# Optimization experiments

Hardware: AMD Instinct MI355X
Metric: run time of the kernel (lower is better)

The kernel has to match this reference:

```python
import jax, jax.numpy as jnp
import numpy as np

N_WIRES = 8
N_LAYERS = 6
OUTPUT_DIM = 8
BATCH = 131072


def _rx(t):
    c = jnp.cos(t / 2).astype(jnp.complex64)
    s = jnp.sin(t / 2).astype(jnp.complex64)
    return jnp.stack([jnp.stack([c, -1j * s], -1), jnp.stack([-1j * s, c], -1)], -2)


def _ry(t):
    c = jnp.cos(t / 2).astype(jnp.complex64)
    s = jnp.sin(t / 2).astype(jnp.complex64)
    return jnp.stack([jnp.stack([c, -s], -1), jnp.stack([s, c], -1)], -2)


def _rz(t):
    e = jnp.exp(-0.5j * t.astype(jnp.complex64))
    z = jnp.zeros_like(e)
    return jnp.stack([jnp.stack([e, z], -1), jnp.stack([z, jnp.conj(e)], -1)], -2)


def _apply_1q(state, U, w):
    # state: [B, 2, 2, ..., 2]; U: [2,2] (shared) or [B,2,2] (per-batch angle)
    s = jnp.moveaxis(state, w + 1, -1)
    if U.ndim == 3:
        s = jnp.einsum('bij,b...j->b...i', U, s)
    else:
        s = jnp.einsum('ij,...j->...i', U, s)
    return jnp.moveaxis(s, -1, w + 1)


def _apply_cnot(state, c, t):
    s = jnp.moveaxis(state, (c + 1, t + 1), (-2, -1))
    s = jnp.concatenate([s[..., :1, :], s[..., 1:, ::-1]], axis=-2)
    return jnp.moveaxis(s, (-2, -1), (c + 1, t + 1))


def _circuit(x, weights):
    B = x.shape[0]
    dim = 2 ** N_WIRES
    state = jnp.zeros((B, dim), dtype=jnp.complex64).at[:, 0].set(1.0)
    state = state.reshape((B,) + (2,) * N_WIRES)
    rx0 = _rx(x[:, 0])  # [B,2,2] data-encoding gates (batched angles)
    ry1 = _ry(x[:, 1])
    for layer in range(N_LAYERS):
        for i in range(N_WIRES):
            state = _apply_1q(state, rx0 if i % 2 == 0 else ry1, i)
        for i in range(N_WIRES):
            state = _apply_1q(state, _rx(weights[layer, i, 0]), i)
            state = _apply_1q(state, _ry(weights[layer, i, 1]), i)
            state = _apply_1q(state, _rz(weights[layer, i, 2]), i)
        for i in range(N_WIRES - 1):
            state = _apply_cnot(state, i, i + 1)
    probs = state.real ** 2 + state.imag ** 2  # [B, 2,...,2]
    evs = []
    for i in range(OUTPUT_DIM):
        p = jnp.moveaxis(probs, i + 1, 1).reshape(B, 2, -1)
        evs.append((p[:, 0] - p[:, 1]).sum(-1))  # <Z_i>
    return jnp.stack(evs, 0)  # [output_dim, B]


def setup_inputs() -> dict:
    key = jax.random.key(0)
    k1, k2 = jax.random.split(key)
    x = jax.random.normal(k1, (BATCH, 2), dtype=jnp.float32)
    weights = jax.random.normal(k2, (N_LAYERS, N_WIRES, 3), dtype=jnp.float32)
    return {'x': x, 'weights': weights}


def reference(x, weights):
    basis_t = _circuit(x, weights) * jnp.pi  # [output_dim, B]
    return basis_t.T  # [B, output_dim]
```

## Files before the change

### kernel.cpp

```cpp
#include <hip/hip_runtime.h>
#include <math.h>

#define N_WIRES 8
#define N_LAYERS 6
#define NG 49
#define NG2 (NG * NG)

#define WS_E_OFF 0
#define WS_FB_OFF 76832

typedef _Float16 half8 __attribute__((ext_vector_type(8)));
typedef float f32x4 __attribute__((ext_vector_type(4)));

__device__ __forceinline__ float row16_sum(float v) {
    v += __int_as_float(__builtin_amdgcn_update_dpp(
        0, __float_as_int(v), 0xB1, 0xF, 0xF, true));
    v += __int_as_float(__builtin_amdgcn_update_dpp(
        0, __float_as_int(v), 0x4E, 0xF, 0xF, true));
    v += __int_as_float(__builtin_amdgcn_update_dpp(
        0, __float_as_int(v), 0x124, 0xF, 0xF, true));
    v += __int_as_float(__builtin_amdgcn_update_dpp(
        0, __float_as_int(v), 0x128, 0xF, 0xF, true));
    return v;
}

__global__ __launch_bounds__(256) void qnn_grid_lds(const float* __restrict__ w,
                                                    float* __restrict__ E) {
    __shared__ float gates[N_LAYERS * N_WIRES * 8];
    __shared__ float2 bufA[256];
    __shared__ float2 bufB[256];
    __shared__ float partial[4][8];

    const int tid = threadIdx.x;
    const int g = blockIdx.x;
    const int ga = (g * 1338) >> 16;
    const int gb = g - ga * NG;
    const float step = (float)(2.0 * M_PI / 49.0);

    if (tid < N_LAYERS * N_WIRES) {
        const int i = tid & 7;
        float wx = w[tid * 3 + 0], wy = w[tid * 3 + 1], wz = w[tid * 3 + 2];
        float sx, cx, sy, cy, sz, cz;
        sincosf(0.5f * wx, &sx, &cx);
        sincosf(0.5f * wy, &sy, &cy);
        sincosf(0.5f * wz, &sz, &cz);
        float A00r = cy * cx, A00i = sy * sx;
        float A01r = -sy * cx, A01i = -cy * sx;
        float A10r = sy * cx, A10i = -cy * sx;
        float A11r = cy * cx, A11i = -sy * sx;
        float U00r = A00r * cz + A00i * sz, U00i = A00i * cz - A00r * sz;
        float U01r = A01r * cz + A01i * sz, U01i = A01i * cz - A01r * sz;
        float U10r = A10r * cz - A10i * sz, U10i = A10i * cz + A10r * sz;
        float U11r = A11r * cz - A11i * sz, U11i = A11i * cz + A11r * sz;
        float V00r, V00i, V01r, V01i, V10r, V10i, V11r, V11i;
        if ((i & 1) == 0) {
            V00r = U01i; V00i = -U01r;
            V01r = U00i; V01i = -U00r;
            V10r = U11i; V10i = -U11r;
            V11r = U10i; V11i = -U10r;
        } else {
            V00r = U01r;  V00i = U01i;
            V01r = -U00r; V01i = -U00i;
            V10r = U11r;  V10i = U11i;
            V11r = -U10r; V11i = -U10i;
        }
        const float xx = (i & 1) ? (step * (float)gb) : (step * (float)ga);
        float se, ce;
        sincosf(0.5f * xx, &se, &ce);
        float* o = gates + tid * 8;
        o[0] = ce * U00r + se * V00r;  o[1] = ce * U00i + se * V00i;
        o[2] = ce * U01r + se * V01r;  o[3] = ce * U01i + se * V01i;
        o[4] = ce * U10r + se * V10r;  o[5] = ce * U10i + se * V10i;
        o[6] = ce * U11r + se * V11r;  o[7] = ce * U11i + se * V11i;
    }

    float ar = (tid == 0) ? 1.0f : 0.0f;
    float ai = 0.0f;
    __syncthreads();

    int flip = 0;
    for (int l = 0; l < N_LAYERS; ++l) {
        #pragma unroll
        for (int i = 0; i < 2; ++i) {
            const float* gm = gates + (l * 8 + i) * 8;
            const int p = 7 - i;
            const int m = 1 << p;
            const int bit = (tid >> p) & 1;
            float2* buf = flip ? bufB : bufA;
            flip ^= 1;
            buf[tid] = make_float2(ar, ai);
            __syncthreads();
            float2 other = buf[tid ^ m];
            float a0r = bit ? other.x : ar, a0i = bit ? other.y : ai;
            float a1r = bit ? ar : other.x, a1i = bit ? ai : other.y;
            float c0r = gm[bit * 4 + 0], c0i = gm[bit * 4 + 1];
            float c1r = gm[bit * 4 + 2], c1i = gm[bit * 4 + 3];
            float nr = c0r * a0r - c0i * a0i + c1r * a1r - c1i * a1i;
            float ni = c0r * a0i + c0i * a0r + c1r * a1i + c1i * a1r;
            ar = nr; ai = ni;
        }
        #pragma unroll
        for (int i = 2; i < 8; ++i) {
            const float* gm = gates + (l * 8 + i) * 8;
            const int p = 7 - i;
            const int m = 1 << p;
            const int bit = (tid >> p) & 1;
            float otr = __shfl_xor(ar, m);
            float oti = __shfl_xor(ai, m);
            float a0r = bit ? otr : ar, a0i = bit ? oti : ai;
            float a1r = bit ? ar : otr, a1i = bit ? ai : oti;
            float c0r = gm[bit * 4 + 0], c0i = gm[bit * 4 + 1];
            float c1r = gm[bit * 4 + 2], c1i = gm[bit * 4 + 3];
            float nr = c0r * a0r - c0i * a0i + c1r * a1r - c1i * a1i;
            float ni = c0r * a0i + c0i * a0r + c1r * a1i + c1i * a1r;
            ar = nr; ai = ni;
        }
        {
            float2* buf = flip ? bufB : bufA;
            flip ^= 1;
            buf[tid] = make_float2(ar, ai);
            __syncthreads();
            float2 src = buf[tid ^ (tid >> 1)];
            ar = src.x; ai = src.y;
        }
    }

    float p = ar * ar + ai * ai;
    float ev[8];
    #pragma unroll
    for (int i = 0; i < 8; ++i) ev[i] = ((tid >> (7 - i)) & 1) ? -p : p;
    #pragma unroll
    for (int i = 0; i < 8; ++i) {
        float v = row16_sum(ev[i]);
        v += __shfl_xor(v, 16);
        v += __shfl_xor(v, 32);
        ev[i] = v;
    }
    const int wave = tid >> 6, lane = tid & 63;
    if (lane == 0) {
        #pragma unroll
        for (int i = 0; i < 8; ++i) partial[wave][i] = ev[i];
    }
    __syncthreads();
    if (tid < 8) {
        E[tid * NG2 + g] = partial[0][tid] + partial[1][tid] + partial[2][tid] + partial[3][tid];
    }
}

__global__ __launch_bounds__(64) void dft2(const float* __restrict__ E,
                                           _Float16* __restrict__ Fb) {
    const int kp = blockIdx.x, i = blockIdx.y, t = threadIdx.x;
    __shared__ float Es[NG2];
    __shared__ float H[NG];
    __shared__ float tc[NG], ts[NG];
    const float step = (float)(2.0 * M_PI / 49.0);
    const float PI = 3.14159265358979323846f;

    if (t < NG) {
        float s, c;
        sincosf(step * (float)t, &s, &c);
        tc[t] = c; ts[t] = s;
    }
    if (kp < NG) {
        for (int e = t; e < NG2; e += 64) Es[e] = E[i * NG2 + e];
    }
    __syncthreads();

    if (kp < NG && t < NG) {
        const int b = t;
        const int n = (kp + 1) >> 1;
        const bool use_cos = (kp & 1) || (kp == 0);
        float acc = 0.f;
        int j = 0;
        for (int a = 0; a < NG; ++a) {
            acc = fmaf(Es[a * NG + b], use_cos ? tc[j] : ts[j], acc);
            j += n; if (j >= NG) j -= NG;
        }
        acc *= (kp == 0) ? (1.0f / 49.0f) : (2.0f / 49.0f);
        H[b] = acc;
    }
    __syncthreads();

    const int l = t;
    float acc = 0.f;
    if (kp < NG && l < NG) {
        const int n = (l + 1) >> 1;
        const bool use_cos = (l & 1) || (l == 0);
        int j = 0;
        for (int b = 0; b < NG; ++b) {
            acc = fmaf(H[b], use_cos ? tc[j] : ts[j], acc);
            j += n; if (j >= NG) j -= NG;
        }
        acc *= (l == 0) ? (PI / 49.0f) : (2.0f * PI / 49.0f);
    }
    {
        const int ntile = kp >> 4, n = kp & 15;
        const int chunk = l >> 5, lrem = l & 31;
        const int q = lrem >> 3, j = lrem & 7;
        const int fid = (i * 4 + ntile) * 2 + chunk;
        Fb[fid * 512 + (q * 16 + n) * 8 + j] = (_Float16)acc;
    }
}

#define V0PAD 68

__global__ __launch_bounds__(256, 4) void contract_mfma(const float* __restrict__ x,
                                                        const _Float16* __restrict__ Fb,
                                                        float* __restrict__ out, int B) {
    __shared__ float xs0[64], xs1[64];
    __shared__ float v0t[64 * V0PAD];
    __shared__ __align__(16) half8 aS[2 * 4 * 64];

    const int tid = threadIdx.x;
    const int bbase = blockIdx.x * 64;
    if (bbase >= B) return;

    const int lane = tid & 63;
    const int w = tid >> 6;
    const int q = lane >> 4;

    const half8* FB = (const half8*)Fb;
    half8 bfrag[16];
    #pragma unroll
    for (int f = 0; f < 16; ++f) bfrag[f] = FB[(w * 16 + f) * 64 + lane];

    if (tid < 64) {
        float2 xv = ((const float2*)x)[bbase + tid];
        xs0[tid] = xv.x;
        xs1[tid] = xv.y;
    }
    __syncthreads();

    {
        const int b = tid & 63, s = tid >> 6;
        const float x0 = xs0[b];
        float c1, s1;
        sincosf(x0, &s1, &c1);
        float s2v = 2.f * s1 * c1, c2v = 1.f - 2.f * s1 * s1;
        float s4v = 2.f * s2v * c2v, c4v = 1.f - 2.f * s2v * s2v;
        float s8v = 2.f * s4v * c4v, c8v = 1.f - 2.f * s4v * s4v;
        float sb, cb;
        if (s == 0) {
            sb = 0.f; cb = 1.f;
        } else if (s == 1) {
            sb = s8v; cb = c8v;
        } else if (s == 2) {
            sb = 2.f * s8v * c8v; cb = 1.f - 2.f * s8v * s8v;
        } else {
            float s16v = 2.f * s8v * c8v, c16v = 1.f - 2.f * s8v * s8v;
            sb = s16v * c8v + c16v * s8v; cb = c16v * c8v - s16v * s8v;
        }
        float* row = v0t + b * V0PAD + 16 * s;
        const int k0 = 16 * s;
        row[0] = (k0 == 0) ? 1.0f : ((k0 < NG) ? sb : 0.0f);
        float cm = cb, sm = sb;
        #pragma unroll
        for (int j = 1; j < 16; ++j) {
            if (j & 1) {
                float c2 = cm * c1 - sm * s1, s2 = sm * c1 + cm * s1;
                cm = c2; sm = s2;
            }
            float val = (j & 1) ? cm : sm;
            row[j] = ((k0 + j) < NG) ? val : 0.0f;
        }
    }

    {
        const float x1v = xs1[w * 16 + (lane & 15)];
        float c1, s1;
        sincosf(x1v, &s1, &c1);
        float s2v = 2.f * s1 * c1, c2v = 1.f - 2.f * s1 * s1;
        float s4v = 2.f * s2v * c2v, c4v = 1.f - 2.f * s2v * s2v;
        float s8v = 2.f * s4v * c4v, c8v = 1.f - 2.f * s4v * s4v;
        float s12v = s8v * c4v + c8v * s4v, c12v = c8v * c4v - s8v * s4v;
        float sq = (q == 0) ? 0.f : ((q == 1) ? s4v : ((q == 2) ? s8v : s12v));
        float cq = (q == 0) ? 1.f : ((q == 1) ? c4v : ((q == 2) ? c8v : c12v));
        float s16v = 2.f * s8v * c8v, c16v = 1.f - 2.f * s8v * s8v;
        float sb_c[2], cb_c[2];
        sb_c[0] = sq;                      cb_c[0] = cq;
        sb_c[1] = sq * c16v + cq * s16v;   cb_c[1] = cq * c16v - sq * s16v;
        #pragma unroll
        for (int c = 0; c < 2; ++c) {
            const int l0 = c * 32 + q * 8;
            float cb = cb_c[c], sb = sb_c[c];
            float vals[8];
            vals[0] = (l0 == 0) ? 1.0f : sb;
            float cm = cb, sm = sb;
            #pragma unroll
            for (int j = 1; j < 8; ++j) {
                if (j & 1) {
                    float c2 = cm * c1 - sm * s1, s2 = sm * c1 + cm * s1;
                    cm = c2; sm = s2;
                }
                vals[j] = (j & 1) ? cm : sm;
            }
            half8 af;
            #pragma unroll
            for (int j = 0; j < 8; ++j) {
                af[j] = (_Float16)(((l0 + j) < 52) ? vals[j] : 0.0f);
            }
            aS[(c * 4 + w) * 64 + lane] = af;
        }
    }

    __syncthreads();

    #pragma unroll 1
    for (int bg = 0; bg < 4; ++bg) {
        const half8 a0 = aS[(0 * 4 + bg) * 64 + lane];
        const half8 a1 = aS[(1 * 4 + bg) * 64 + lane];

        float res[2][4];
        #pragma unroll
        for (int ii = 0; ii < 2; ++ii)
            #pragma unroll
            for (int r = 0; r < 4; ++r) res[ii][r] = 0.f;

        #pragma unroll
        for (int nt = 0; nt < 4; ++nt) {
            float v0[4];
            #pragma unroll
            for (int r = 0; r < 4; ++r)
                v0[r] = v0t[(bg * 16 + q * 4 + r) * V0PAD + nt * 16 + (lane & 15)];

            f32x4 z = {0.f, 0.f, 0.f, 0.f};
            f32x4 acc0 = __builtin_amdgcn_mfma_f32_16x16x32_f16(a0, bfrag[nt * 2 + 0], z, 0, 0, 0);
            acc0 = __builtin_amdgcn_mfma_f32_16x16x32_f16(a1, bfrag[nt * 2 + 1], acc0, 0, 0, 0);
            f32x4 acc1 = __builtin_amdgcn_mfma_f32_16x16x32_f16(a0, bfrag[(4 + nt) * 2 + 0], z, 0, 0, 0);
            acc1 = __builtin_amdgcn_mfma_f32_16x16x32_f16(a1, bfrag[(4 + nt) * 2 + 1], acc1, 0, 0, 0);

            #pragma unroll
            for (int r = 0; r < 4; ++r) {
                res[0][r] = fmaf(acc0[r], v0[r], res[0][r]);
                res[1][r] = fmaf(acc1[r], v0[r], res[1][r]);
            }
        }

        #pragma unroll
        for (int ii = 0; ii < 2; ++ii)
            #pragma unroll
            for (int r = 0; r < 4; ++r) {
                res[ii][r] = row16_sum(res[ii][r]);
            }

        if ((lane & 15) == 0) {
            #pragma unroll
            for (int r = 0; r < 4; ++r) {
                const int b = bbase + bg * 16 + q * 4 + r;
                float2 st = make_float2(res[0][r], res[1][r]);
                *(float2*)&out[(size_t)b * 8 + 2 * w] = st;
            }
        }
    }
}

extern "C" void kernel_launch(void* const* d_in, const int* in_sizes, int n_in,
                              void* d_out, int out_size, void* d_ws, size_t ws_size,
                              hipStream_t stream) {
    (void)n_in; (void)out_size; (void)ws_size;
    const float* x = (const float*)d_in[0];
    const float* w = (const float*)d_in[1];
    float* out = (float*)d_out;
    char* ws = (char*)d_ws;
    float* E = (float*)(ws + WS_E_OFF);
    _Float16* Fb = (_Float16*)(ws + WS_FB_OFF);
    const int B = in_sizes[0] / 2;

    hipLaunchKernelGGL(qnn_grid_lds, dim3(NG2), dim3(256), 0, stream, w, E);
    hipLaunchKernelGGL(dft2, dim3(64, 8), dim3(64), 0, stream, E, Fb);
    hipLaunchKernelGGL(contract_mfma, dim3((B + 63) / 64, 1), dim3(256), 0, stream,
                       x, Fb, out, B);
}
```

Baseline: 96.16 us.

## Absorb CNOT permutations into gate index masks and split DFT reductions across waves

The CNOT ladder at the end of each layer is no longer applied as an LDS permutation with a barrier. It is folded into per-layer partner masks and parity masks, computed with popc, and into sign masks for the final Z expectations. This removes six LDS round-trips and syncs per circuit block. The dft2 kernel now uses 256 threads and splits each 49-term sum across four waves with an LDS partial reduction, to shorten the serial loops. Gate coefficients are also read with a float4 load. These changes add index arithmetic and extra barriers in dft2.

Measured after the change: 96.31 us. Within noise of the previous version (+0.2%).

```diff
diff --git a/kernel.cpp b/kernel.cpp
--- a/kernel.cpp
+++ b/kernel.cpp
@@ -23,6 +23,25 @@
         0, __float_as_int(v), 0x128, 0xF, 0xF, true));
     return v;
 }
+
+static __device__ constexpr unsigned char MGATE[6][8] = {
+    {0x80, 0x40, 0x20, 0x10, 0x08, 0x04, 0x02, 0x01},
+    {0xC0, 0x60, 0x30, 0x18, 0x0C, 0x06, 0x03, 0x01},
+    {0xA0, 0x50, 0x28, 0x14, 0x0A, 0x05, 0x02, 0x01},
+    {0xF0, 0x78, 0x3C, 0x1E, 0x0F, 0x07, 0x03, 0x01},
+    {0x88, 0x44, 0x22, 0x11, 0x08, 0x04, 0x02, 0x01},
+    {0xCC, 0x66, 0x33, 0x19, 0x0C, 0x06, 0x03, 0x01},
+};
+static __device__ constexpr unsigned char RGATE[6][8] = {
+    {0x80, 0x40, 0x20, 0x10, 0x08, 0x04, 0x02, 0x01},
+    {0x80, 0xC0, 0xE0, 0xF0, 0xF8, 0xFC, 0xFE, 0xFF},
+    {0x80, 0x40, 0xA0, 0x50, 0xA8, 0x54, 0xAA, 0x55},
+    {0x80, 0xC0, 0x60, 0x30, 0x98, 0xCC, 0x66, 0x33},
+    {0x80, 0x40, 0x20, 0x10, 0x88, 0x44, 0x22, 0x11},
+    {0x80, 0xC0, 0xE0, 0xF0, 0x78, 0x3C, 0x1E, 0x0F},
+};
+static __device__ constexpr unsigned char SMASK[8] =
+    {0x80, 0x40, 0xA0, 0x50, 0x28, 0x14, 0x0A, 0x05};
 
 __global__ __launch_bounds__(256) void qnn_grid_lds(const float* __restrict__ w,
                                                     float* __restrict__ E) {
@@ -79,13 +98,13 @@
     __syncthreads();
 
     int flip = 0;
+    #pragma unroll
     for (int l = 0; l < N_LAYERS; ++l) {
         #pragma unroll
         for (int i = 0; i < 2; ++i) {
             const float* gm = gates + (l * 8 + i) * 8;
-            const int p = 7 - i;
-            const int m = 1 << p;
-            const int bit = (tid >> p) & 1;
+            const int m = MGATE[l][i];
+            const int bit = __popc(tid & RGATE[l][i]) & 1;
             float2* buf = flip ? bufB : bufA;
             flip ^= 1;
             buf[tid] = make_float2(ar, ai);
@@ -93,42 +112,32 @@
             float2 other = buf[tid ^ m];
             float a0r = bit ? other.x : ar, a0i = bit ? other.y : ai;
             float a1r = bit ? ar : other.x, a1i = bit ? ai : other.y;
-            float c0r = gm[bit * 4 + 0], c0i = gm[bit * 4 + 1];
-            float c1r = gm[bit * 4 + 2], c1i = gm[bit * 4 + 3];
-            float nr = c0r * a0r - c0i * a0i + c1r * a1r - c1i * a1i;
-            float ni = c0r * a0i + c0i * a0r + c1r * a1i + c1i * a1r;
+            float4 cc = *(const float4*)(gm + bit * 4);
+            float nr = cc.x * a0r - cc.y * a0i + cc.z * a1r - cc.w * a1i;
+            float ni = cc.x * a0i + cc.y * a0r + cc.z * a1i + cc.w * a1r;
             ar = nr; ai = ni;
         }
         #pragma unroll
         for (int i = 2; i < 8; ++i) {
             const float* gm = gates + (l * 8 + i) * 8;
-            const int p = 7 - i;
-            const int m = 1 << p;
-            const int bit = (tid >> p) & 1;
+            const int m = MGATE[l][i];
+            const int bit = __popc(tid & RGATE[l][i]) & 1;
             float otr = __shfl_xor(ar, m);
             float oti = __shfl_xor(ai, m);
             float a0r = bit ? otr : ar, a0i = bit ? oti : ai;
             float a1r = bit ? ar : otr, a1i = bit ? ai : oti;
-            float c0r = gm[bit * 4 + 0], c0i = gm[bit * 4 + 1];
-            float c1r = gm[bit * 4 + 2], c1i = gm[bit * 4 + 3];
-            float nr = c0r * a0r - c0i * a0i + c1r * a1r - c1i * a1i;
-            float ni = c0r * a0i + c0i * a0r + c1r * a1i + c1i * a1r;
+            float4 cc = *(const float4*)(gm + bit * 4);
+            float nr = cc.x * a0r - cc.y * a0i + cc.z * a1r - cc.w * a1i;
+            float ni = cc.x * a0i + cc.y * a0r + cc.z * a1i + cc.w * a1r;
             ar = nr; ai = ni;
-        }
-        {
-            float2* buf = flip ? bufB : bufA;
-            flip ^= 1;
-            buf[tid] = make_float2(ar, ai);
-            __syncthreads();
-            float2 src = buf[tid ^ (tid >> 1)];
-            ar = src.x; ai = src.y;
         }
     }
 
     float p = ar * ar + ai * ai;
     float ev[8];
     #pragma unroll
-    for (int i = 0; i < 8; ++i) ev[i] = ((tid >> (7 - i)) & 1) ? -p : p;
+    for (int i = 0; i < 8; ++i)
+        ev[i] = (__popc(tid & SMASK[i]) & 1) ? -p : p;
     #pragma unroll
     for (int i = 0; i < 8; ++i) {
         float v = row16_sum(ev[i]);
@@ -147,12 +156,15 @@
     }
 }
 
-__global__ __launch_bounds__(64) void dft2(const float* __restrict__ E,
-                                           _Float16* __restrict__ Fb) {
-    const int kp = blockIdx.x, i = blockIdx.y, t = threadIdx.x;
+__global__ __launch_bounds__(256) void dft2(const float* __restrict__ E,
+                                            _Float16* __restrict__ Fb) {
+    const int kp = blockIdx.x, i = blockIdx.y;
+    const int t = threadIdx.x, w = t >> 6, lane = t & 63;
     __shared__ float Es[NG2];
+    __shared__ float tc[NG], ts[NG];
+    __shared__ float Hp[4][NG + 3];
     __shared__ float H[NG];
-    __shared__ float tc[NG], ts[NG];
+    __shared__ float Fp[4][64];
     const float step = (float)(2.0 * M_PI / 49.0);
     const float PI = 3.14159265358979323846f;
 
@@ -161,39 +173,51 @@
         sincosf(step * (float)t, &s, &c);
         tc[t] = c; ts[t] = s;
     }
-    if (kp < NG) {
-        for (int e = t; e < NG2; e += 64) Es[e] = E[i * NG2 + e];
-    }
-    __syncthreads();
-
-    if (kp < NG && t < NG) {
-        const int b = t;
+    for (int e = t; e < NG2; e += 256) Es[e] = E[i * NG2 + e];
+    __syncthreads();
+
+    if (kp < NG && lane < NG) {
+        const int a0 = w * 13, a1 = (a0 + 13 < NG) ? a0 + 13 : NG;
         const int n = (kp + 1) >> 1;
         const bool use_cos = (kp & 1) || (kp == 0);
         float acc = 0.f;
-        int j = 0;
-        for (int a = 0; a < NG; ++a) {
-            acc = fmaf(Es[a * NG + b], use_cos ? tc[j] : ts[j], acc);
+        int j = (a0 * n) % NG;
+        for (int a = a0; a < a1; ++a) {
+            acc = fmaf(Es[a * NG + lane], use_cos ? tc[j] : ts[j], acc);
             j += n; if (j >= NG) j -= NG;
         }
-        acc *= (kp == 0) ? (1.0f / 49.0f) : (2.0f / 49.0f);
-        H[b] = acc;
-    }
-    __syncthreads();
-
-    const int l = t;
-    float acc = 0.f;
-    if (kp < NG && l < NG) {
-        const int n = (l + 1) >> 1;
-        const bool use_cos = (l & 1) || (l == 0);
-        int j = 0;
-        for (int b = 0; b < NG; ++b) {
-            acc = fmaf(H[b], use_cos ? tc[j] : ts[j], acc);
-            j += n; if (j >= NG) j -= NG;
-        }
+        Hp[w][lane] = acc;
+    }
+    __syncthreads();
+
+    if (t < NG) {
+        float h = ((Hp[0][t] + Hp[1][t]) + Hp[2][t]) + Hp[3][t];
+        h *= (kp == 0) ? (1.0f / 49.0f) : (2.0f / 49.0f);
+        H[t] = h;
+    }
+    __syncthreads();
+
+    {
+        float acc = 0.f;
+        if (kp < NG && lane < NG) {
+            const int b0 = w * 13, b1 = (b0 + 13 < NG) ? b0 + 13 : NG;
+            const int n = (lane + 1) >> 1;
+            const bool use_cos = (lane & 1) || (lane == 0);
+            int j = (b0 * n) % NG;
+            for (int b = b0; b < b1; ++b) {
+                acc = fmaf(H[b], use_cos ? tc[j] : ts[j], acc);
+                j += n; if (j >= NG) j -= NG;
+            }
+        }
+        Fp[w][lane] = acc;
+    }
+    __syncthreads();
+
+    if (t < 64) {
+        const int l = t;
+        float acc = ((Fp[0][l] + Fp[1][l]) + Fp[2][l]) + Fp[3][l];
         acc *= (l == 0) ? (PI / 49.0f) : (2.0f * PI / 49.0f);
-    }
-    {
+        if (kp >= NG || l >= NG) acc = 0.f;
         const int ntile = kp >> 4, n = kp & 15;
         const int chunk = l >> 5, lrem = l & 31;
         const int q = lrem >> 3, j = lrem & 7;
@@ -367,7 +391,7 @@
     const int B = in_sizes[0] / 2;
 
     hipLaunchKernelGGL(qnn_grid_lds, dim3(NG2), dim3(256), 0, stream, w, E);
-    hipLaunchKernelGGL(dft2, dim3(64, 8), dim3(64), 0, stream, E, Fb);
+    hipLaunchKernelGGL(dft2, dim3(64, 8), dim3(256), 0, stream, E, Fb);
     hipLaunchKernelGGL(contract_mfma, dim3((B + 63) / 64, 1), dim3(256), 0, stream,
                        x, Fb, out, B);
 }
```
